# Kernel tuning notes

Hardware: AMD Instinct MI355X
Metric: run time of the kernel (lower is better)

Reference implementation:

```python
import jax, jax.numpy as jnp
import numpy as np
import math

B, T, DIM, NH = 2, 2048, 2048, 16
HD = DIM // NH  # 128


def rotate_half(x):
    h = x.shape[-1] // 2
    return jnp.concatenate([-x[..., h:], x[..., :h]], axis=-1)


def rope_tables(t_len, rot_dim, base=10000.0, dtype=jnp.float32):
    # rot_dim = head_dim; inv_freq has rot_dim//2 entries -> sin/cos [T, rot_dim//2]
    inv_freq = 1.0 / (base ** (jnp.arange(0, rot_dim, 2, dtype=dtype) / rot_dim))
    t = jnp.arange(t_len, dtype=dtype)
    ang = jnp.einsum('i,j->ij', t, inv_freq)  # [T, rot_dim//2]
    return jnp.sin(ang), jnp.cos(ang)


def apply_rope(q, k, sin, cos):
    # Partial RoPE as in source: rotate only the first half of head_dim,
    # using sin/cos of width head_dim//2 matched to that half.
    h = q.shape[-1] // 2
    q1, q2 = q[..., :h], q[..., h:]
    k1, k2 = k[..., :h], k[..., h:]
    sin = sin[None, None]  # [1,1,T,h]
    cos = cos[None, None]
    q1r = q1 * cos + rotate_half(q1) * sin
    k1r = k1 * cos + rotate_half(k1) * sin
    return jnp.concatenate([q1r, q2], axis=-1), jnp.concatenate([k1r, k2], axis=-1)


def setup_inputs() -> dict:
    key = jax.random.key(0)
    ks = jax.random.split(key, 5)
    s = 1.0 / math.sqrt(DIM)
    return {
        'x': jax.random.normal(ks[0], (B, T, DIM), jnp.float32),
        'wq': jax.random.normal(ks[1], (DIM, DIM), jnp.float32) * s,
        'wk': jax.random.normal(ks[2], (DIM, DIM), jnp.float32) * s,
        'wv': jax.random.normal(ks[3], (DIM, DIM), jnp.float32) * s,
        'wo': jax.random.normal(ks[4], (DIM, DIM), jnp.float32) * s,
    }


def reference(x, wq, wk, wv, wo):
    b, t, c = x.shape
    def proj(w):
        return (x @ w.T).reshape(b, t, NH, HD).transpose(0, 2, 1, 3)  # [B,H,T,hd]
    q, k, v = proj(wq), proj(wk), proj(wv)
    sin, cos = rope_tables(t, HD, dtype=x.dtype)
    q, k = apply_rope(q, k, sin, cos)
    att = jnp.einsum('bhqd,bhkd->bhqk', q, k) * (1.0 / math.sqrt(HD))  # [B,H,T,T]
    att = jax.nn.softmax(att, axis=-1)
    y = jnp.einsum('bhqk,bhkd->bhqd', att, v)
    y = y.transpose(0, 2, 1, 3).reshape(b, t, c)
    return y @ wo.T
```

## Files before the change

kernel.cpp:

```cpp
#include <hip/hip_runtime.h>

typedef unsigned short u16;
typedef __attribute__((ext_vector_type(4))) u16 u16x4;
typedef __attribute__((ext_vector_type(8))) __bf16 bf16x8;
typedef __attribute__((ext_vector_type(4))) float f32x4;

#define B_ 2
#define T_ 2048
#define DIM_ 2048
#define NH_ 16
#define HD_ 128

__device__ __forceinline__ u16 f2b(float f) {
  unsigned u = __builtin_bit_cast(unsigned, f);
  u += 0x7fffu + ((u >> 16) & 1u);
  return (u16)(u >> 16);
}
__device__ __forceinline__ float b2f(u16 h) {
  unsigned u = ((unsigned)h) << 16;
  return __builtin_bit_cast(float, u);
}

typedef __attribute__((address_space(1))) void gvoid_t;
typedef __attribute__((address_space(3))) void lvoid_t;
__device__ __forceinline__ void gload16(const void* g, void* l) {
  __builtin_amdgcn_global_load_lds((gvoid_t*)g, (lvoid_t*)l, 16, 0, 0);
}

__global__ __launch_bounds__(256) void cvt_bf16(const float* x, const float* wq,
    const float* wk, const float* wv, const float* wo,
    u16* xb, u16* wqb, u16* wkb, u16* wvb, u16* wob) {
  int ten = blockIdx.y;
  const float* s; u16* d; int n4;
  if (ten == 0)      { s = x;  d = xb;  n4 = 2097152; }
  else if (ten == 1) { s = wq; d = wqb; n4 = 1048576; }
  else if (ten == 2) { s = wk; d = wkb; n4 = 1048576; }
  else if (ten == 3) { s = wv; d = wvb; n4 = 1048576; }
  else               { s = wo; d = wob; n4 = 1048576; }
  int i = blockIdx.x * 256 + threadIdx.x;
  if (i >= n4) return;
  float4 f = ((const float4*)s)[i];
  u16x4 o = { f2b(f.x), f2b(f.y), f2b(f.z), f2b(f.w) };
  ((u16x4*)d)[i] = o;
}

template <typename OutT>
__device__ __forceinline__ void gemm_bt_body(const u16* A, const u16* Bw, OutT* C) {
  constexpr int K = 2048, N = 2048;
  __shared__ u16 As[128 * 32];
  __shared__ u16 Bs[128 * 32];
  const int tid = threadIdx.x;
  const int w = tid >> 6, l = tid & 63, n = l & 15, quad = l >> 4;
  const int row0 = blockIdx.y * 128, col0 = blockIdx.x * 128;
  const int c = w * 64 + l;
  const int rA = c >> 2, kA = (c & 3) * 8;
  const u16* aP1 = A + (size_t)(row0 + rA) * K + kA;
  const u16* aP2 = A + (size_t)(row0 + 64 + rA) * K + kA;
  const u16* bP1 = Bw + (size_t)(col0 + rA) * K + kA;
  const u16* bP2 = Bw + (size_t)(col0 + 64 + rA) * K + kA;
  char* lA1 = (char*)As + (w * 64) * 16;
  char* lA2 = (char*)As + (256 + w * 64) * 16;
  char* lB1 = (char*)Bs + (w * 64) * 16;
  char* lB2 = (char*)Bs + (256 + w * 64) * 16;
  const int wr0 = (w >> 1) * 64, wc0 = (w & 1) * 64;
  f32x4 acc[4][4] = {};
  for (int kt = 0; kt < K; kt += 32) {
    gload16(aP1, lA1); gload16(aP2, lA2);
    gload16(bP1, lB1); gload16(bP2, lB2);
    aP1 += 32; aP2 += 32; bP1 += 32; bP2 += 32;
    __syncthreads();
    bf16x8 af[4], bfr[4];
#pragma unroll
    for (int mb = 0; mb < 4; ++mb)
      af[mb] = *(const bf16x8*)&As[(wr0 + mb * 16 + n) * 32 + quad * 8];
#pragma unroll
    for (int nb = 0; nb < 4; ++nb)
      bfr[nb] = *(const bf16x8*)&Bs[(wc0 + nb * 16 + n) * 32 + quad * 8];
#pragma unroll
    for (int mb = 0; mb < 4; ++mb)
#pragma unroll
      for (int nb = 0; nb < 4; ++nb)
        acc[mb][nb] = __builtin_amdgcn_mfma_f32_16x16x32_bf16(af[mb], bfr[nb], acc[mb][nb], 0, 0, 0);
    __syncthreads();
  }
#pragma unroll
  for (int mb = 0; mb < 4; ++mb)
#pragma unroll
    for (int nb = 0; nb < 4; ++nb)
#pragma unroll
      for (int r = 0; r < 4; ++r) {
        size_t idx = (size_t)(row0 + wr0 + mb * 16 + quad * 4 + r) * N + (col0 + wc0 + nb * 16 + n);
        float v = acc[mb][nb][r];
        if constexpr (sizeof(OutT) == 2) C[idx] = f2b(v); else C[idx] = v;
      }
}

__global__ __launch_bounds__(256) void gemm_qkv(const u16* A, const u16* w0, const u16* w1,
    const u16* w2, u16* c0, u16* c1, u16* c2) {
  const u16* Bw = (blockIdx.z == 0) ? w0 : (blockIdx.z == 1) ? w1 : w2;
  u16* C = (blockIdx.z == 0) ? c0 : (blockIdx.z == 1) ? c1 : c2;
  gemm_bt_body<u16>(A, Bw, C);
}
__global__ __launch_bounds__(256) void gemm_o(const u16* A, const u16* Bw, float* C) {
  gemm_bt_body<float>(A, Bw, C);
}

__global__ __launch_bounds__(256) void rope_k(u16* Qb, u16* Kb) {
  int gid = blockIdx.x * 256 + threadIdx.x;
  int j = gid & 31;
  int h = (gid >> 5) & 15;
  int row = gid >> 9;
  int t = row & (T_ - 1);
  bool isQ = (blockIdx.y == 0);
  u16* base = (isQ ? Qb : Kb) + (size_t)row * DIM_ + h * HD_;
  double f1 = exp2(-(double)j * 0.20762050593045951);
  double f2 = f1 * 0.01;
  const double INV2PI = 0.15915494309189535;
  double r1d = (double)t * f1 * INV2PI; r1d -= floor(r1d);
  double r2d = (double)t * f2 * INV2PI; r2d -= floor(r2d);
  float rv1 = (float)r1d, rv2 = (float)r2d;
  float c1 = __builtin_amdgcn_cosf(rv1), s1 = __builtin_amdgcn_sinf(rv1);
  float c2 = __builtin_amdgcn_cosf(rv2), s2 = __builtin_amdgcn_sinf(rv2);
  float x1 = b2f(base[j]), x2 = b2f(base[j + 32]);
  float scale = isQ ? 0.12751743342408354f : 1.0f;
  base[j]      = f2b((x1 * c1 - x2 * s1) * scale);
  base[j + 32] = f2b((x2 * c2 + x1 * s2) * scale);
  if (isQ) {
    base[j + 64] = f2b(b2f(base[j + 64]) * scale);
    base[j + 96] = f2b(b2f(base[j + 96]) * scale);
  }
}

__global__ __launch_bounds__(256) void transpose_v(const u16* V, u16* Vt) {
  int b = blockIdx.z;
  int t0 = blockIdx.x * 64, c0 = blockIdx.y * 64;
  __shared__ u16 tile[64][72];
  int tid = threadIdx.x;
#pragma unroll
  for (int i = 0; i < 4; ++i) {
    int v = i * 256 + tid;
    int r = v >> 4, c4 = (v & 15) * 4;
    *(u16x4*)&tile[r][c4] = *(const u16x4*)(V + (size_t)(b * T_ + t0 + r) * DIM_ + c0 + c4);
  }
  __syncthreads();
#pragma unroll
  for (int i = 0; i < 4; ++i) {
    int v = i * 256 + tid;
    int d = v >> 4, t4 = (v & 15) * 4;
    u16x4 o = { tile[t4 + 0][d], tile[t4 + 1][d], tile[t4 + 2][d], tile[t4 + 3][d] };
    *(u16x4*)(Vt + (size_t)(b * DIM_ + c0 + d) * T_ + t0 + t4) = o;
  }
}

__global__ __launch_bounds__(256, 1) void attn_k(const u16* Q, const u16* K, const u16* Vt, u16* Y) {
  const int qt = blockIdx.x, bh = blockIdx.y;
  const int b = bh >> 4, h = bh & 15;
  const int tid = threadIdx.x;
  const int w = tid >> 6, l = tid & 63, n = l & 15, quad = l >> 4;
  __shared__ u16 Ks[128 * 128];
  __shared__ u16 Vs[2][128 * 128];
  __shared__ u16 Ps[128 * 136];

  const u16* Qbase = Q + (size_t)(b * T_ + qt * 128) * DIM_ + h * HD_;
  const u16* Kbase = K + (size_t)(b * T_) * DIM_ + h * HD_;
  const u16* Vbase = Vt + (size_t)(b * DIM_ + h * HD_) * T_;

  const int wr0 = w * 32;
  bf16x8 qf[2][4];
#pragma unroll
  for (int mb = 0; mb < 2; ++mb)
#pragma unroll
    for (int s = 0; s < 4; ++s)
      qf[mb][s] = *(const bf16x8*)(Qbase + (size_t)(wr0 + mb * 16 + n) * DIM_ + s * 32 + quad * 8);

  auto stage = [&](const u16* rowbase, u16* lds) {
#pragma unroll
    for (int inst = 0; inst < 8; ++inst) {
      int ci = inst * 256 + w * 64 + l;
      int r = ci >> 4, cl = ci & 15;
      int cg = cl ^ (4 * (r & 3));
      gload16(rowbase + (size_t)r * 2048 + cg * 8, (char*)lds + (inst * 256 + w * 64) * 16);
    }
  };

  stage(Kbase, Ks);
  stage(Vbase, Vs[0]);
  f32x4 o[2][8] = {};
  float m_r[2][4], l_r[2][4];
#pragma unroll
  for (int mb = 0; mb < 2; ++mb)
#pragma unroll
    for (int r = 0; r < 4; ++r) { m_r[mb][r] = -__builtin_inff(); l_r[mb][r] = 0.f; }

  for (int it = 0; it < 16; ++it) {
    __syncthreads();
    if (it + 1 < 16) stage(Vbase + (it + 1) * 128, Vs[(it + 1) & 1]);

    f32x4 s_[2][8] = {};
#pragma unroll
    for (int ks = 0; ks < 4; ++ks) {
      bf16x8 kf[8];
#pragma unroll
      for (int nb = 0; nb < 8; ++nb)
        kf[nb] = *(const bf16x8*)&Ks[(nb * 16 + n) * 128 + (((ks * 4 + quad) ^ (4 * (n & 3))) * 8)];
#pragma unroll
      for (int mb = 0; mb < 2; ++mb)
#pragma unroll
        for (int nb = 0; nb < 8; ++nb)
          s_[mb][nb] = __builtin_amdgcn_mfma_f32_16x16x32_bf16(qf[mb][ks], kf[nb], s_[mb][nb], 0, 0, 0);
    }

#pragma unroll
    for (int mb = 0; mb < 2; ++mb)
#pragma unroll
      for (int r = 0; r < 4; ++r) {
        float mx = s_[mb][0][r];
#pragma unroll
        for (int nb = 1; nb < 8; ++nb) mx = fmaxf(mx, s_[mb][nb][r]);
        mx = fmaxf(mx, __shfl_xor(mx, 1, 64));
        mx = fmaxf(mx, __shfl_xor(mx, 2, 64));
        mx = fmaxf(mx, __shfl_xor(mx, 4, 64));
        mx = fmaxf(mx, __shfl_xor(mx, 8, 64));
        float mo = m_r[mb][r];
        float mn = fmaxf(mo, mx);
        float al = __builtin_amdgcn_exp2f(mo - mn);
        float rs = 0.f;
#pragma unroll
        for (int nb = 0; nb < 8; ++nb) {
          float p = __builtin_amdgcn_exp2f(s_[mb][nb][r] - mn);
          s_[mb][nb][r] = p;
          rs += p;
        }
        rs += __shfl_xor(rs, 1, 64);
        rs += __shfl_xor(rs, 2, 64);
        rs += __shfl_xor(rs, 4, 64);
        rs += __shfl_xor(rs, 8, 64);
        l_r[mb][r] = al * l_r[mb][r] + rs;
        m_r[mb][r] = mn;
#pragma unroll
        for (int nb = 0; nb < 8; ++nb) o[mb][nb][r] *= al;
      }

#pragma unroll
    for (int mb = 0; mb < 2; ++mb)
#pragma unroll
      for (int nb = 0; nb < 8; ++nb)
#pragma unroll
        for (int r = 0; r < 4; ++r)
          Ps[(wr0 + mb * 16 + quad * 4 + r) * 136 + nb * 16 + n] = f2b(s_[mb][nb][r]);
    __syncthreads();
    if (it + 1 < 16) stage(Kbase + (size_t)((it + 1) * 128) * 2048, Ks);

    const u16* Vsc = Vs[it & 1];
#pragma unroll
    for (int ks = 0; ks < 4; ++ks) {
      bf16x8 pa[2];
#pragma unroll
      for (int mb = 0; mb < 2; ++mb)
        pa[mb] = *(const bf16x8*)&Ps[(wr0 + mb * 16 + n) * 136 + ks * 32 + quad * 8];
      bf16x8 vf[8];
#pragma unroll
      for (int nb = 0; nb < 8; ++nb)
        vf[nb] = *(const bf16x8*)&Vsc[(nb * 16 + n) * 128 + (((ks * 4 + quad) ^ (4 * (n & 3))) * 8)];
#pragma unroll
      for (int mb = 0; mb < 2; ++mb)
#pragma unroll
        for (int nb = 0; nb < 8; ++nb)
          o[mb][nb] = __builtin_amdgcn_mfma_f32_16x16x32_bf16(pa[mb], vf[nb], o[mb][nb], 0, 0, 0);
    }
  }

  u16* Ybase = Y + (size_t)(b * T_ + qt * 128) * DIM_ + h * HD_;
#pragma unroll
  for (int mb = 0; mb < 2; ++mb)
#pragma unroll
    for (int r = 0; r < 4; ++r) {
      float inv = 1.0f / l_r[mb][r];
#pragma unroll
      for (int nb = 0; nb < 8; ++nb)
        Ybase[(size_t)(wr0 + mb * 16 + quad * 4 + r) * DIM_ + nb * 16 + n] = f2b(o[mb][nb][r] * inv);
    }
}

extern "C" void kernel_launch(void* const* d_in, const int* in_sizes, int n_in,
                              void* d_out, int out_size, void* d_ws, size_t ws_size,
                              hipStream_t stream) {
  const float* x  = (const float*)d_in[0];
  const float* wq = (const float*)d_in[1];
  const float* wk = (const float*)d_in[2];
  const float* wv = (const float*)d_in[3];
  const float* wo = (const float*)d_in[4];

  u16* ws  = (u16*)d_ws;
  u16* xb  = ws;
  u16* wqb = xb + 8388608;
  u16* wkb = wqb + 4194304;
  u16* wvb = wkb + 4194304;
  u16* wob = wvb + 4194304;
  u16* qb  = wob + 4194304;
  u16* kb  = qb + 8388608;
  u16* vb  = kb + 8388608;
  u16* vt  = vb + 8388608;
  u16* yb  = vt + 8388608;

  cvt_bf16<<<dim3(8192, 5), 256, 0, stream>>>(x, wq, wk, wv, wo, xb, wqb, wkb, wvb, wob);
  gemm_qkv<<<dim3(16, 32, 3), 256, 0, stream>>>(xb, wqb, wkb, wvb, qb, kb, vb);
  rope_k<<<dim3(8192, 2), 256, 0, stream>>>(qb, kb);
  transpose_v<<<dim3(32, 32, 2), 256, 0, stream>>>(vb, vt);
  attn_k<<<dim3(16, 32), 256, 0, stream>>>(qb, kb, vt, yb);
  gemm_o<<<dim3(16, 32), 256, 0, stream>>>(yb, wob, (float*)d_out);
}
```

Before: 471.8 us.

## Compute transposed S and O tiles to keep P in registers, dropping LDS staging

The attention kernel now swaps the MFMA operand order so each lane holds a query column of S^T and O^T. Softmax row reductions become cross-quad shuffles, and the bf16 P fragment for the PV MFMA is assembled with register shuffles instead of a round trip through an LDS P buffer. V is now single-buffered, which frees enough LDS to raise launch bounds to two blocks per CU. In exchange, the K/V prefetch of the next tile no longer overlaps compute across iterations as it did before, and more barriers are added.

```diff
diff --git a/kernel.cpp b/kernel.cpp
--- a/kernel.cpp
+++ b/kernel.cpp
@@ -19,6 +19,9 @@
 __device__ __forceinline__ float b2f(u16 h) {
   unsigned u = ((unsigned)h) << 16;
   return __builtin_bit_cast(float, u);
+}
+__device__ __forceinline__ unsigned pack2(float lo, float hi) {
+  return (unsigned)f2b(lo) | ((unsigned)f2b(hi) << 16);
 }
 
 typedef __attribute__((address_space(1))) void gvoid_t;
@@ -152,26 +155,24 @@
   }
 }
 
-__global__ __launch_bounds__(256, 1) void attn_k(const u16* Q, const u16* K, const u16* Vt, u16* Y) {
+__global__ __launch_bounds__(256, 2) void attn_k(const u16* Q, const u16* K, const u16* Vt, u16* Y) {
   const int qt = blockIdx.x, bh = blockIdx.y;
   const int b = bh >> 4, h = bh & 15;
   const int tid = threadIdx.x;
   const int w = tid >> 6, l = tid & 63, n = l & 15, quad = l >> 4;
   __shared__ u16 Ks[128 * 128];
-  __shared__ u16 Vs[2][128 * 128];
-  __shared__ u16 Ps[128 * 136];
-
-  const u16* Qbase = Q + (size_t)(b * T_ + qt * 128) * DIM_ + h * HD_;
+  __shared__ u16 Vs[128 * 128];
+
+  const u16* Qbase = Q + (size_t)(b * T_ + qt * 128 + w * 32) * DIM_ + h * HD_;
   const u16* Kbase = K + (size_t)(b * T_) * DIM_ + h * HD_;
   const u16* Vbase = Vt + (size_t)(b * DIM_ + h * HD_) * T_;
 
-  const int wr0 = w * 32;
   bf16x8 qf[2][4];
 #pragma unroll
-  for (int mb = 0; mb < 2; ++mb)
-#pragma unroll
-    for (int s = 0; s < 4; ++s)
-      qf[mb][s] = *(const bf16x8*)(Qbase + (size_t)(wr0 + mb * 16 + n) * DIM_ + s * 32 + quad * 8);
+  for (int qtile = 0; qtile < 2; ++qtile)
+#pragma unroll
+    for (int ks = 0; ks < 4; ++ks)
+      qf[qtile][ks] = *(const bf16x8*)(Qbase + (size_t)(qtile * 16 + n) * DIM_ + ks * 32 + quad * 8);
 
   auto stage = [&](const u16* rowbase, u16* lds) {
 #pragma unroll
@@ -184,102 +185,116 @@
   };
 
   stage(Kbase, Ks);
-  stage(Vbase, Vs[0]);
+  stage(Vbase, Vs);
+
   f32x4 o[2][8] = {};
-  float m_r[2][4], l_r[2][4];
-#pragma unroll
-  for (int mb = 0; mb < 2; ++mb)
-#pragma unroll
-    for (int r = 0; r < 4; ++r) { m_r[mb][r] = -__builtin_inff(); l_r[mb][r] = 0.f; }
+  float m_r[2] = { -__builtin_inff(), -__builtin_inff() };
+  float l_r[2] = { 0.f, 0.f };
+
+  const int shA = ((quad & 1) * 2) * 16 + n;
+  const int shB = shA + 16;
+  const bool hiTile = (quad >= 2);
 
   for (int it = 0; it < 16; ++it) {
     __syncthreads();
-    if (it + 1 < 16) stage(Vbase + (it + 1) * 128, Vs[(it + 1) & 1]);
-
-    f32x4 s_[2][8] = {};
+
+    f32x4 st[2][8] = {};
 #pragma unroll
     for (int ks = 0; ks < 4; ++ks) {
       bf16x8 kf[8];
 #pragma unroll
-      for (int nb = 0; nb < 8; ++nb)
-        kf[nb] = *(const bf16x8*)&Ks[(nb * 16 + n) * 128 + (((ks * 4 + quad) ^ (4 * (n & 3))) * 8)];
-#pragma unroll
-      for (int mb = 0; mb < 2; ++mb)
-#pragma unroll
-        for (int nb = 0; nb < 8; ++nb)
-          s_[mb][nb] = __builtin_amdgcn_mfma_f32_16x16x32_bf16(qf[mb][ks], kf[nb], s_[mb][nb], 0, 0, 0);
-    }
-
-#pragma unroll
-    for (int mb = 0; mb < 2; ++mb)
-#pragma unroll
-      for (int r = 0; r < 4; ++r) {
-        float mx = s_[mb][0][r];
-#pragma unroll
-        for (int nb = 1; nb < 8; ++nb) mx = fmaxf(mx, s_[mb][nb][r]);
-        mx = fmaxf(mx, __shfl_xor(mx, 1, 64));
-        mx = fmaxf(mx, __shfl_xor(mx, 2, 64));
-        mx = fmaxf(mx, __shfl_xor(mx, 4, 64));
-        mx = fmaxf(mx, __shfl_xor(mx, 8, 64));
-        float mo = m_r[mb][r];
-        float mn = fmaxf(mo, mx);
-        float al = __builtin_amdgcn_exp2f(mo - mn);
-        float rs = 0.f;
-#pragma unroll
-        for (int nb = 0; nb < 8; ++nb) {
-          float p = __builtin_amdgcn_exp2f(s_[mb][nb][r] - mn);
-          s_[mb][nb][r] = p;
+      for (int mt = 0; mt < 8; ++mt)
+        kf[mt] = *(const bf16x8*)&Ks[(mt * 16 + n) * 128 + (((ks * 4 + quad) ^ (4 * (n & 3))) * 8)];
+#pragma unroll
+      for (int qtile = 0; qtile < 2; ++qtile)
+#pragma unroll
+        for (int mt = 0; mt < 8; ++mt)
+          st[qtile][mt] = __builtin_amdgcn_mfma_f32_16x16x32_bf16(kf[mt], qf[qtile][ks], st[qtile][mt], 0, 0, 0);
+    }
+    __syncthreads();
+    if (it + 1 < 16) stage(Kbase + (size_t)((it + 1) * 128) * 2048, Ks);
+
+    unsigned pk[2][8][2];
+#pragma unroll
+    for (int qtile = 0; qtile < 2; ++qtile) {
+      float mx = -__builtin_inff();
+#pragma unroll
+      for (int mt = 0; mt < 8; ++mt)
+#pragma unroll
+        for (int r = 0; r < 4; ++r) mx = fmaxf(mx, st[qtile][mt][r]);
+      mx = fmaxf(mx, __shfl_xor(mx, 16, 64));
+      mx = fmaxf(mx, __shfl_xor(mx, 32, 64));
+      float mo = m_r[qtile];
+      float mn = fmaxf(mo, mx);
+      float al = __builtin_amdgcn_exp2f(mo - mn);
+      float rs = 0.f;
+#pragma unroll
+      for (int mt = 0; mt < 8; ++mt)
+#pragma unroll
+        for (int r = 0; r < 4; ++r) {
+          float p = __builtin_amdgcn_exp2f(st[qtile][mt][r] - mn);
+          st[qtile][mt][r] = p;
           rs += p;
         }
-        rs += __shfl_xor(rs, 1, 64);
-        rs += __shfl_xor(rs, 2, 64);
-        rs += __shfl_xor(rs, 4, 64);
-        rs += __shfl_xor(rs, 8, 64);
-        l_r[mb][r] = al * l_r[mb][r] + rs;
-        m_r[mb][r] = mn;
-#pragma unroll
-        for (int nb = 0; nb < 8; ++nb) o[mb][nb][r] *= al;
+      rs += __shfl_xor(rs, 16, 64);
+      rs += __shfl_xor(rs, 32, 64);
+      l_r[qtile] = al * l_r[qtile] + rs;
+      m_r[qtile] = mn;
+#pragma unroll
+      for (int mt = 0; mt < 8; ++mt) {
+        pk[qtile][mt][0] = pack2(st[qtile][mt][0], st[qtile][mt][1]);
+        pk[qtile][mt][1] = pack2(st[qtile][mt][2], st[qtile][mt][3]);
       }
-
-#pragma unroll
-    for (int mb = 0; mb < 2; ++mb)
-#pragma unroll
-      for (int nb = 0; nb < 8; ++nb)
-#pragma unroll
-        for (int r = 0; r < 4; ++r)
-          Ps[(wr0 + mb * 16 + quad * 4 + r) * 136 + nb * 16 + n] = f2b(s_[mb][nb][r]);
-    __syncthreads();
-    if (it + 1 < 16) stage(Kbase + (size_t)((it + 1) * 128) * 2048, Ks);
-
-    const u16* Vsc = Vs[it & 1];
+#pragma unroll
+      for (int mt = 0; mt < 8; ++mt)
+#pragma unroll
+        for (int r = 0; r < 4; ++r) o[qtile][mt][r] *= al;
+    }
+
+    typedef __attribute__((ext_vector_type(4))) unsigned uint4v;
+    uint4v pT[2][4];
+#pragma unroll
+    for (int qtile = 0; qtile < 2; ++qtile)
+#pragma unroll
+      for (int ks = 0; ks < 4; ++ks) {
+#pragma unroll
+        for (int jj = 0; jj < 4; ++jj) {
+          int src = (jj < 2) ? shA : shB;
+          unsigned vA = __shfl((int)pk[qtile][ks * 2][jj & 1], src, 64);
+          unsigned vB = __shfl((int)pk[qtile][ks * 2 + 1][jj & 1], src, 64);
+          pT[qtile][ks][jj] = hiTile ? vB : vA;
+        }
+      }
+
 #pragma unroll
     for (int ks = 0; ks < 4; ++ks) {
-      bf16x8 pa[2];
-#pragma unroll
-      for (int mb = 0; mb < 2; ++mb)
-        pa[mb] = *(const bf16x8*)&Ps[(wr0 + mb * 16 + n) * 136 + ks * 32 + quad * 8];
       bf16x8 vf[8];
 #pragma unroll
-      for (int nb = 0; nb < 8; ++nb)
-        vf[nb] = *(const bf16x8*)&Vsc[(nb * 16 + n) * 128 + (((ks * 4 + quad) ^ (4 * (n & 3))) * 8)];
-#pragma unroll
-      for (int mb = 0; mb < 2; ++mb)
-#pragma unroll
-        for (int nb = 0; nb < 8; ++nb)
-          o[mb][nb] = __builtin_amdgcn_mfma_f32_16x16x32_bf16(pa[mb], vf[nb], o[mb][nb], 0, 0, 0);
-    }
-  }
-
-  u16* Ybase = Y + (size_t)(b * T_ + qt * 128) * DIM_ + h * HD_;
-#pragma unroll
-  for (int mb = 0; mb < 2; ++mb)
-#pragma unroll
-    for (int r = 0; r < 4; ++r) {
-      float inv = 1.0f / l_r[mb][r];
-#pragma unroll
-      for (int nb = 0; nb < 8; ++nb)
-        Ybase[(size_t)(wr0 + mb * 16 + quad * 4 + r) * DIM_ + nb * 16 + n] = f2b(o[mb][nb][r] * inv);
-    }
+      for (int mt = 0; mt < 8; ++mt)
+        vf[mt] = *(const bf16x8*)&Vs[(mt * 16 + n) * 128 + (((ks * 4 + quad) ^ (4 * (n & 3))) * 8)];
+#pragma unroll
+      for (int qtile = 0; qtile < 2; ++qtile) {
+        bf16x8 pfrag = __builtin_bit_cast(bf16x8, pT[qtile][ks]);
+#pragma unroll
+        for (int mt = 0; mt < 8; ++mt)
+          o[qtile][mt] = __builtin_amdgcn_mfma_f32_16x16x32_bf16(vf[mt], pfrag, o[qtile][mt], 0, 0, 0);
+      }
+    }
+    __syncthreads();
+    if (it + 1 < 16) stage(Vbase + (it + 1) * 128, Vs);
+  }
+
+  u16* Ybase = Y + (size_t)(b * T_ + qt * 128 + w * 32) * DIM_ + h * HD_;
+#pragma unroll
+  for (int qtile = 0; qtile < 2; ++qtile) {
+    float inv = 1.0f / l_r[qtile];
+#pragma unroll
+    for (int mt = 0; mt < 8; ++mt) {
+      u16x4 ov = { f2b(o[qtile][mt][0] * inv), f2b(o[qtile][mt][1] * inv),
+                   f2b(o[qtile][mt][2] * inv), f2b(o[qtile][mt][3] * inv) };
+      *(u16x4*)(Ybase + (size_t)(qtile * 16 + n) * DIM_ + mt * 16 + quad * 4) = ov;
+    }
+  }
 }
 
 extern "C" void kernel_launch(void* const* d_in, const int* in_sizes, int n_in,
```

After: 441.2 us. 1.07x faster.
